# Kernel optimization log

Measured on AMD Instinct MI355X. Metric: run time of the kernel, lower is better.

The kernel has to match this reference:

```python
import jax, jax.numpy as jnp
import numpy as np

N, C, D, Q, G = 262144, 72, 256, 128, 3  # points, in_channels, hidden, queries, heads
EPS_LN = 1e-5


def _ln(x, g, b):
    m = jnp.mean(x, axis=-1, keepdims=True)
    v = jnp.mean(jnp.square(x - m), axis=-1, keepdims=True)
    return (x - m) * jax.lax.rsqrt(v + EPS_LN) * g + b


def _normalize(x):
    n = jnp.linalg.norm(x, axis=-1, keepdims=True)
    return x / jnp.maximum(n, 1e-12)


def setup_inputs() -> dict:
    key = jax.random.key(0)
    ks = iter(jax.random.split(key, 32))
    r = lambda *s: (jax.random.normal(next(ks), s, dtype=jnp.float32) * 0.02)
    inp = {
        'point_feat': jax.random.normal(next(ks), (N, C), dtype=jnp.float32),
        # input_proj: Linear(C,D) -> LN -> GELU -> Linear(D,D)
        'ip_w1': r(C, D), 'ip_b1': r(D), 'ip_ln_g': jnp.ones((D,), jnp.float32),
        'ip_ln_b': jnp.zeros((D,), jnp.float32), 'ip_w2': r(D, D), 'ip_b2': r(D),
        # point_head: LN -> Linear -> GELU -> Linear
        'ph_ln_g': jnp.ones((D,), jnp.float32), 'ph_ln_b': jnp.zeros((D,), jnp.float32),
        'ph_w1': r(D, D), 'ph_b1': r(D), 'ph_w2': r(D, D), 'ph_b2': r(D),
        # per-head params stacked on leading G axis
        'qe': r(G, Q, D),
        'qh_ln_g': jnp.ones((G, D), jnp.float32), 'qh_ln_b': jnp.zeros((G, D), jnp.float32),
        'qh_w1': r(G, D, D), 'qh_b1': r(G, D), 'qh_w2': r(G, D, D), 'qh_b2': r(G, D),
        'sh_ln_g': jnp.ones((G, D), jnp.float32), 'sh_ln_b': jnp.zeros((G, D), jnp.float32),
        'sh_w1': r(G, D, D), 'sh_b1': r(G, D), 'sh_w2': r(G, D, 1), 'sh_b2': r(G, 1),
        'logit_scale': jnp.full((G,), np.log(10.0), dtype=jnp.float32),
    }
    return inp


def reference(point_feat, ip_w1, ip_b1, ip_ln_g, ip_ln_b, ip_w2, ip_b2,
              ph_ln_g, ph_ln_b, ph_w1, ph_b1, ph_w2, ph_b2,
              qe, qh_ln_g, qh_ln_b, qh_w1, qh_b1, qh_w2, qh_b2,
              sh_ln_g, sh_ln_b, sh_w1, sh_b1, sh_w2, sh_b2, logit_scale):
    gelu = lambda x: jax.nn.gelu(x, approximate=False)  # torch nn.GELU default (erf)
    # shared trunk
    h = gelu(_ln(point_feat @ ip_w1 + ip_b1, ip_ln_g, ip_ln_b)) @ ip_w2 + ip_b2  # [N,D]
    point_embed = h + (gelu(_ln(h, ph_ln_g, ph_ln_b) @ ph_w1 + ph_b1) @ ph_w2 + ph_b2)
    # per-head query MLP (vectorized over G)
    qh = _ln(qe, qh_ln_g[:, None, :], qh_ln_b[:, None, :])
    qh = gelu(jnp.einsum('gqd,gde->gqe', qh, qh_w1) + qh_b1[:, None, :])
    query_embed = qe + jnp.einsum('gqd,gde->gqe', qh, qh_w2) + qh_b2[:, None, :]  # [G,Q,D]
    # scaled cosine-similarity cross-attention (normalize_mask_embeddings=True)
    pmask = _normalize(point_embed)                      # [N,D]
    qmask = _normalize(query_embed)                      # [G,Q,D]
    scale = jnp.exp(logit_scale)[:, None, None]
    mask_logits = scale * jnp.einsum('gqd,nd->gqn', qmask, pmask)   # [G,Q,N]
    mask_weights = jax.nn.softmax(mask_logits, axis=-1)
    pooled = jnp.einsum('gqn,nd->gqd', mask_weights, point_embed)
    refined = query_embed + pooled                       # [G,Q,D]
    # score head
    sh = _ln(refined, sh_ln_g[:, None, :], sh_ln_b[:, None, :])
    sh = gelu(jnp.einsum('gqd,gde->gqe', sh, sh_w1) + sh_b1[:, None, :])
    score_logits = (jnp.einsum('gqd,gdo->gqo', sh, sh_w2) + sh_b2[:, None, :])[..., 0]  # [G,Q]
    return point_embed, mask_logits, score_logits, refined
```

## Files before the change

kernel.cpp:

```cpp
#include <hip/hip_runtime.h>
#include <math.h>

#define NPTS 262144
#define CIN  72
#define DIM  256

typedef _Float16 h8v __attribute__((ext_vector_type(8)));
typedef _Float16 h4v __attribute__((ext_vector_type(4)));
typedef float    f4v __attribute__((ext_vector_type(4)));

__device__ __forceinline__ float gelu_erf(float x) {
    return 0.5f * x * (1.0f + erff(x * 0.70710678118654752440f));
}

__global__ void prep_kernel(const float* __restrict__ w1, const float* __restrict__ w2,
                            const float* __restrict__ p1, const float* __restrict__ p2,
                            _Float16* __restrict__ WT1, _Float16* __restrict__ WT2,
                            _Float16* __restrict__ WTp1, _Float16* __restrict__ WTp2,
                            float* __restrict__ sumexp, float* __restrict__ pooled)
{
    int idx = blockIdx.x * 256 + threadIdx.x;
    if (idx < 24576) {
        int n = idx / 96, k = idx - n * 96;
        WT1[idx] = (_Float16)(k < CIN ? w1[k * DIM + n] : 0.0f);
    } else if (idx < 24576 + 65536) {
        int t = idx - 24576; int n = t >> 8, k = t & 255;
        WT2[t] = (_Float16)w2[k * DIM + n];
    } else if (idx < 24576 + 131072) {
        int t = idx - (24576 + 65536); int n = t >> 8, k = t & 255;
        WTp1[t] = (_Float16)p1[k * DIM + n];
    } else if (idx < 24576 + 196608) {
        int t = idx - (24576 + 131072); int n = t >> 8, k = t & 255;
        WTp2[t] = (_Float16)p2[k * DIM + n];
    } else if (idx < 24576 + 196608 + 384) {
        sumexp[idx - (24576 + 196608)] = 0.0f;
    } else if (idx < 24576 + 196608 + 384 + 98304) {
        pooled[idx - (24576 + 196608 + 384)] = 0.0f;
    }
}

__device__ __forceinline__ float block_sum256(float v, float* s4) {
    #pragma unroll
    for (int off = 1; off < 64; off <<= 1) v += __shfl_xor(v, off, 64);
    __syncthreads();
    if ((threadIdx.x & 63) == 0) s4[threadIdx.x >> 6] = v;
    __syncthreads();
    return s4[0] + s4[1] + s4[2] + s4[3];
}

__global__ __launch_bounds__(256) void query_kernel(
    const float* __restrict__ qe, const float* __restrict__ qg, const float* __restrict__ qb,
    const float* __restrict__ qw1, const float* __restrict__ qb1,
    const float* __restrict__ qw2, const float* __restrict__ qb2,
    float* __restrict__ qemb, _Float16* __restrict__ qmask)
{
    __shared__ float sv[DIM], s2[DIM], s4[4];
    const int row = blockIdx.x, g = row >> 7, d = threadIdx.x;
    const float* w1 = qw1 + (size_t)g * DIM * DIM;
    const float* w2 = qw2 + (size_t)g * DIM * DIM;
    float x = qe[row * DIM + d];
    float mean = block_sum256(x, s4) * (1.0f / DIM);
    float dv = x - mean;
    float var = block_sum256(dv * dv, s4) * (1.0f / DIM);
    float y = dv * rsqrtf(var + 1e-5f) * qg[g * DIM + d] + qb[g * DIM + d];
    sv[d] = y;
    __syncthreads();
    float a1 = 0.0f;
    for (int k = 0; k < DIM; ++k) a1 += sv[k] * w1[k * DIM + d];
    a1 = gelu_erf(a1 + qb1[g * DIM + d]);
    s2[d] = a1;
    __syncthreads();
    float a2 = 0.0f;
    for (int k = 0; k < DIM; ++k) a2 += s2[k] * w2[k * DIM + d];
    float q2 = x + a2 + qb2[g * DIM + d];
    qemb[row * DIM + d] = q2;
    float ss = block_sum256(q2 * q2, s4);
    float inv = 1.0f / fmaxf(sqrtf(ss), 1e-12f);
    qmask[row * DIM + d] = (_Float16)(q2 * inv);
}

__device__ __forceinline__ void zero_acc44(f4v (&acc)[4][4]) {
    #pragma unroll
    for (int m = 0; m < 4; ++m)
        #pragma unroll
        for (int n = 0; n < 4; ++n) {
            f4v z = {0.0f, 0.0f, 0.0f, 0.0f};
            acc[m][n] = z;
        }
}

__device__ __forceinline__ void mm_tile(f4v (&acc)[4][4], const _Float16* sA,
                                        const _Float16* __restrict__ WT, int wtStride,
                                        int nKt, int cb, int l15, int lg)
{
    for (int kt = 0; kt < nKt; ++kt) {
        h8v a[4], b[4];
        #pragma unroll
        for (int m = 0; m < 4; ++m)
            a[m] = *(const h8v*)(sA + (m * 16 + l15) * 264 + kt * 32 + lg * 8);
        #pragma unroll
        for (int n = 0; n < 4; ++n)
            b[n] = *(const h8v*)(WT + (size_t)(cb + n * 16 + l15) * wtStride + kt * 32 + lg * 8);
        #pragma unroll
        for (int m = 0; m < 4; ++m)
            #pragma unroll
            for (int n = 0; n < 4; ++n)
                acc[m][n] = __builtin_amdgcn_mfma_f32_16x16x32_f16(a[m], b[n], acc[m][n], 0, 0, 0);
    }
}

__device__ __forceinline__ void ln_stats(const f4v (&acc)[4][4],
                                         float (*sRed)[64][2], float (*sStat)[2],
                                         int wv, int l15, int lg, int tid)
{
    #pragma unroll
    for (int m = 0; m < 4; ++m) {
        float s[4] = {0, 0, 0, 0}, ss[4] = {0, 0, 0, 0};
        #pragma unroll
        for (int n = 0; n < 4; ++n)
            #pragma unroll
            for (int i = 0; i < 4; ++i) { float v = acc[m][n][i]; s[i] += v; ss[i] += v * v; }
        #pragma unroll
        for (int off = 1; off < 16; off <<= 1)
            #pragma unroll
            for (int i = 0; i < 4; ++i) {
                s[i] += __shfl_xor(s[i], off, 64);
                ss[i] += __shfl_xor(ss[i], off, 64);
            }
        if (l15 == 0)
            #pragma unroll
            for (int i = 0; i < 4; ++i) {
                int r = m * 16 + lg * 4 + i;
                sRed[wv][r][0] = s[i]; sRed[wv][r][1] = ss[i];
            }
    }
    __syncthreads();
    if (tid < 64) {
        float s = 0, ss = 0;
        #pragma unroll
        for (int w = 0; w < 4; ++w) { s += sRed[w][tid][0]; ss += sRed[w][tid][1]; }
        float mean = s * (1.0f / 256.0f);
        float var = ss * (1.0f / 256.0f) - mean * mean;
        sStat[tid][0] = mean;
        sStat[tid][1] = rsqrtf(var + 1e-5f);
    }
    __syncthreads();
}

__global__ __launch_bounds__(256, 2) void trunk_kernel(
    const float* __restrict__ pf,
    const float* __restrict__ ib1, const float* __restrict__ ig, const float* __restrict__ ibb,
    const float* __restrict__ ib2,
    const float* __restrict__ pg, const float* __restrict__ pb,
    const float* __restrict__ pb1, const float* __restrict__ pb2,
    const _Float16* __restrict__ WT1, const _Float16* __restrict__ WT2,
    const _Float16* __restrict__ WTp1, const _Float16* __restrict__ WTp2,
    float* __restrict__ peo, float* __restrict__ inv_norm, _Float16* __restrict__ peT)
{
    __shared__ __align__(16) _Float16 sAct[64][264];
    __shared__ float sRed[4][64][2];
    __shared__ float sStat[64][2];

    const int tid = threadIdx.x;
    const int wv = tid >> 6, ln = tid & 63, l15 = ln & 15, lg = ln >> 4;
    const int cb = wv * 64;
    const int rowbase = blockIdx.x * 64;

    for (int idx = tid; idx < 64 * 96; idx += 256) {
        int r = idx / 96, c = idx - r * 96;
        sAct[r][c] = (_Float16)(c < CIN ? pf[(size_t)(rowbase + r) * CIN + c] : 0.0f);
    }
    __syncthreads();

    f4v acc[4][4];
    float h4[4][4][4];

    zero_acc44(acc);
    mm_tile(acc, &sAct[0][0], WT1, 96, 3, cb, l15, lg);
    {
        float bc[4], gc[4], bb[4];
        #pragma unroll
        for (int n = 0; n < 4; ++n) {
            int col = cb + n * 16 + l15;
            bc[n] = ib1[col]; gc[n] = ig[col]; bb[n] = ibb[col];
        }
        #pragma unroll
        for (int m = 0; m < 4; ++m)
            #pragma unroll
            for (int n = 0; n < 4; ++n)
                #pragma unroll
                for (int i = 0; i < 4; ++i) acc[m][n][i] += bc[n];
        ln_stats(acc, sRed, sStat, wv, l15, lg, tid);
        #pragma unroll
        for (int m = 0; m < 4; ++m)
            #pragma unroll
            for (int i = 0; i < 4; ++i) {
                int r = m * 16 + lg * 4 + i;
                float mean = sStat[r][0], rstd = sStat[r][1];
                #pragma unroll
                for (int n = 0; n < 4; ++n) {
                    float v = (acc[m][n][i] - mean) * rstd * gc[n] + bb[n];
                    sAct[r][cb + n * 16 + l15] = (_Float16)gelu_erf(v);
                }
            }
    }
    __syncthreads();

    zero_acc44(acc);
    mm_tile(acc, &sAct[0][0], WT2, 256, 8, cb, l15, lg);
    {
        float bc[4], gc[4], bb[4];
        #pragma unroll
        for (int n = 0; n < 4; ++n) {
            int col = cb + n * 16 + l15;
            bc[n] = ib2[col]; gc[n] = pg[col]; bb[n] = pb[col];
        }
        #pragma unroll
        for (int m = 0; m < 4; ++m)
            #pragma unroll
            for (int n = 0; n < 4; ++n)
                #pragma unroll
                for (int i = 0; i < 4; ++i) {
                    float h = acc[m][n][i] + bc[n];
                    h4[m][n][i] = h;
                    acc[m][n][i] = h;
                }
        ln_stats(acc, sRed, sStat, wv, l15, lg, tid);
        #pragma unroll
        for (int m = 0; m < 4; ++m)
            #pragma unroll
            for (int i = 0; i < 4; ++i) {
                int r = m * 16 + lg * 4 + i;
                float mean = sStat[r][0], rstd = sStat[r][1];
                #pragma unroll
                for (int n = 0; n < 4; ++n) {
                    float v = (h4[m][n][i] - mean) * rstd * gc[n] + bb[n];
                    sAct[r][cb + n * 16 + l15] = (_Float16)v;
                }
            }
    }
    __syncthreads();

    zero_acc44(acc);
    mm_tile(acc, &sAct[0][0], WTp1, 256, 8, cb, l15, lg);
    __syncthreads();
    {
        float bc[4];
        #pragma unroll
        for (int n = 0; n < 4; ++n) bc[n] = pb1[cb + n * 16 + l15];
        #pragma unroll
        for (int m = 0; m < 4; ++m)
            #pragma unroll
            for (int i = 0; i < 4; ++i) {
                int r = m * 16 + lg * 4 + i;
                #pragma unroll
                for (int n = 0; n < 4; ++n) {
                    float v = gelu_erf(acc[m][n][i] + bc[n]);
                    sAct[r][cb + n * 16 + l15] = (_Float16)v;
                }
            }
    }
    __syncthreads();

    zero_acc44(acc);
    mm_tile(acc, &sAct[0][0], WTp2, 256, 8, cb, l15, lg);
    {
        float bc[4];
        #pragma unroll
        for (int n = 0; n < 4; ++n) bc[n] = pb2[cb + n * 16 + l15];
        #pragma unroll
        for (int m = 0; m < 4; ++m)
            #pragma unroll
            for (int n = 0; n < 4; ++n)
                #pragma unroll
                for (int i = 0; i < 4; ++i)
                    acc[m][n][i] += bc[n] + h4[m][n][i];
        #pragma unroll
        for (int m = 0; m < 4; ++m) {
            float ss[4] = {0, 0, 0, 0};
            #pragma unroll
            for (int n = 0; n < 4; ++n)
                #pragma unroll
                for (int i = 0; i < 4; ++i) { float v = acc[m][n][i]; ss[i] += v * v; }
            #pragma unroll
            for (int off = 1; off < 16; off <<= 1)
                #pragma unroll
                for (int i = 0; i < 4; ++i) ss[i] += __shfl_xor(ss[i], off, 64);
            if (l15 == 0)
                #pragma unroll
                for (int i = 0; i < 4; ++i) sRed[wv][m * 16 + lg * 4 + i][0] = ss[i];
        }
        __syncthreads();
        if (tid < 64) {
            float ss = 0;
            #pragma unroll
            for (int w = 0; w < 4; ++w) ss += sRed[w][tid][0];
            float inv = 1.0f / fmaxf(sqrtf(ss), 1e-12f);
            sStat[tid][0] = inv;
            inv_norm[rowbase + tid] = inv;
        }
        __syncthreads();
        #pragma unroll
        for (int m = 0; m < 4; ++m)
            #pragma unroll
            for (int n = 0; n < 4; ++n) {
                int col = cb + n * 16 + l15;
                h4v pk;
                #pragma unroll
                for (int i = 0; i < 4; ++i) {
                    int r = m * 16 + lg * 4 + i;
                    float v = acc[m][n][i];
                    peo[(size_t)(rowbase + r) * DIM + col] = v;
                    pk[i] = (_Float16)v;
                }
                *(h4v*)(peT + (size_t)col * NPTS + rowbase + m * 16 + lg * 4) = pk;
            }
    }
}

__global__ __launch_bounds__(256, 2) void logits_kernel(
    const _Float16* __restrict__ qmask, const float* __restrict__ peo,
    const float* __restrict__ inv_norm, const float* __restrict__ lsc,
    float* __restrict__ ml, float* __restrict__ sumexp)
{
    const int tid = threadIdx.x;
    const int wv = tid >> 6, ln = tid & 63, l15 = ln & 15, lg = ln >> 4;
    const int nb = blockIdx.x * 64;
    const int mb = wv * 96;

    f4v acc[6][4];
    #pragma unroll
    for (int m = 0; m < 6; ++m)
        #pragma unroll
        for (int n = 0; n < 4; ++n) { f4v z = {0, 0, 0, 0}; acc[m][n] = z; }

    float inv[4];
    #pragma unroll
    for (int n = 0; n < 4; ++n) inv[n] = inv_norm[nb + n * 16 + l15];

    for (int kt = 0; kt < 8; ++kt) {
        h8v a[6], b[4];
        #pragma unroll
        for (int n = 0; n < 4; ++n) {
            const float* p = peo + (size_t)(nb + n * 16 + l15) * DIM + kt * 32 + lg * 8;
            float4 u0 = *(const float4*)p;
            float4 u1 = *(const float4*)(p + 4);
            h8v t;
            t[0] = (_Float16)(u0.x * inv[n]); t[1] = (_Float16)(u0.y * inv[n]);
            t[2] = (_Float16)(u0.z * inv[n]); t[3] = (_Float16)(u0.w * inv[n]);
            t[4] = (_Float16)(u1.x * inv[n]); t[5] = (_Float16)(u1.y * inv[n]);
            t[6] = (_Float16)(u1.z * inv[n]); t[7] = (_Float16)(u1.w * inv[n]);
            b[n] = t;
        }
        #pragma unroll
        for (int m = 0; m < 6; ++m)
            a[m] = *(const h8v*)(qmask + (size_t)(mb + m * 16 + l15) * DIM + kt * 32 + lg * 8);
        #pragma unroll
        for (int m = 0; m < 6; ++m)
            #pragma unroll
            for (int n = 0; n < 4; ++n)
                acc[m][n] = __builtin_amdgcn_mfma_f32_16x16x32_f16(a[m], b[n], acc[m][n], 0, 0, 0);
    }

    #pragma unroll
    for (int m = 0; m < 6; ++m) {
        int g = (mb + m * 16) >> 7;
        float sc = expf(lsc[g]);
        float es[4] = {0, 0, 0, 0};
        #pragma unroll
        for (int n = 0; n < 4; ++n)
            #pragma unroll
            for (int i = 0; i < 4; ++i) {
                int row = mb + m * 16 + lg * 4 + i;
                int col = nb + n * 16 + l15;
                float v = acc[m][n][i] * sc;
                ml[(size_t)row * NPTS + col] = v;
                es[i] += __expf(v);
            }
        #pragma unroll
        for (int off = 1; off < 16; off <<= 1)
            #pragma unroll
            for (int i = 0; i < 4; ++i) es[i] += __shfl_xor(es[i], off, 64);
        if (l15 == 0)
            #pragma unroll
            for (int i = 0; i < 4; ++i)
                atomicAdd(&sumexp[mb + m * 16 + lg * 4 + i], es[i]);
    }
}

__global__ __launch_bounds__(512, 2) void pooled_kernel(
    const float* __restrict__ ml, const _Float16* __restrict__ peT,
    float* __restrict__ pooled)
{
    const int tid = threadIdx.x;
    const int wv = tid >> 6, ln = tid & 63, l15 = ln & 15, lg = ln >> 4;
    const int mt = blockIdx.x >> 7, kc = blockIdx.x & 127;
    const int mb = mt * 192 + (wv & 3) * 48;
    const int cbv = (wv >> 2) * 128;
    const size_t kb = (size_t)kc * 2048;

    f4v acc[3][8];
    #pragma unroll
    for (int m = 0; m < 3; ++m)
        #pragma unroll
        for (int n = 0; n < 8; ++n) { f4v z = {0, 0, 0, 0}; acc[m][n] = z; }

    for (int ks = 0; ks < 64; ++ks) {
        size_t k0 = kb + ks * 32 + lg * 8;
        h8v a[3];
        #pragma unroll
        for (int m = 0; m < 3; ++m) {
            const float* p = ml + (size_t)(mb + m * 16 + l15) * NPTS + k0;
            float4 u0 = *(const float4*)p;
            float4 u1 = *(const float4*)(p + 4);
            h8v t;
            t[0] = (_Float16)__expf(u0.x); t[1] = (_Float16)__expf(u0.y);
            t[2] = (_Float16)__expf(u0.z); t[3] = (_Float16)__expf(u0.w);
            t[4] = (_Float16)__expf(u1.x); t[5] = (_Float16)__expf(u1.y);
            t[6] = (_Float16)__expf(u1.z); t[7] = (_Float16)__expf(u1.w);
            a[m] = t;
        }
        h8v b[8];
        #pragma unroll
        for (int n = 0; n < 8; ++n)
            b[n] = *(const h8v*)(peT + (size_t)(cbv + n * 16 + l15) * NPTS + k0);
        #pragma unroll
        for (int m = 0; m < 3; ++m)
            #pragma unroll
            for (int n = 0; n < 8; ++n)
                acc[m][n] = __builtin_amdgcn_mfma_f32_16x16x32_f16(a[m], b[n], acc[m][n], 0, 0, 0);
    }
    #pragma unroll
    for (int m = 0; m < 3; ++m)
        #pragma unroll
        for (int n = 0; n < 8; ++n)
            #pragma unroll
            for (int i = 0; i < 4; ++i)
                atomicAdd(&pooled[(mb + m * 16 + lg * 4 + i) * DIM + cbv + n * 16 + l15],
                          acc[m][n][i]);
}

__global__ __launch_bounds__(256) void finalize_kernel(
    const float* __restrict__ pooled, const float* __restrict__ sumexp,
    const float* __restrict__ qemb,
    const float* __restrict__ sg, const float* __restrict__ sb,
    const float* __restrict__ sw1, const float* __restrict__ sb1,
    const float* __restrict__ sw2, const float* __restrict__ sb2,
    float* __restrict__ rf, float* __restrict__ sl)
{
    __shared__ float sv[DIM], s4[4];
    const int row = blockIdx.x, g = row >> 7, d = threadIdx.x;
    float r = qemb[row * DIM + d] + pooled[row * DIM + d] / sumexp[row];
    rf[row * DIM + d] = r;
    float mean = block_sum256(r, s4) * (1.0f / DIM);
    float dv = r - mean;
    float var = block_sum256(dv * dv, s4) * (1.0f / DIM);
    float y = dv * rsqrtf(var + 1e-5f) * sg[g * DIM + d] + sb[g * DIM + d];
    sv[d] = y;
    __syncthreads();
    const float* w1 = sw1 + (size_t)g * DIM * DIM;
    float a1 = 0.0f;
    for (int k = 0; k < DIM; ++k) a1 += sv[k] * w1[k * DIM + d];
    a1 = gelu_erf(a1 + sb1[g * DIM + d]);
    float part = a1 * sw2[g * DIM + d];
    float tot = block_sum256(part, s4);
    if (d == 0) sl[row] = tot + sb2[g];
}

extern "C" void kernel_launch(void* const* d_in, const int* in_sizes, int n_in,
                              void* d_out, int out_size, void* d_ws, size_t ws_size,
                              hipStream_t stream) {
    const float* pf       = (const float*)d_in[0];
    const float* ip_w1    = (const float*)d_in[1];
    const float* ip_b1    = (const float*)d_in[2];
    const float* ip_ln_g  = (const float*)d_in[3];
    const float* ip_ln_b  = (const float*)d_in[4];
    const float* ip_w2    = (const float*)d_in[5];
    const float* ip_b2    = (const float*)d_in[6];
    const float* ph_ln_g  = (const float*)d_in[7];
    const float* ph_ln_b  = (const float*)d_in[8];
    const float* ph_w1    = (const float*)d_in[9];
    const float* ph_b1    = (const float*)d_in[10];
    const float* ph_w2    = (const float*)d_in[11];
    const float* ph_b2    = (const float*)d_in[12];
    const float* qe       = (const float*)d_in[13];
    const float* qh_ln_g  = (const float*)d_in[14];
    const float* qh_ln_b  = (const float*)d_in[15];
    const float* qh_w1    = (const float*)d_in[16];
    const float* qh_b1    = (const float*)d_in[17];
    const float* qh_w2    = (const float*)d_in[18];
    const float* qh_b2    = (const float*)d_in[19];
    const float* sh_ln_g  = (const float*)d_in[20];
    const float* sh_ln_b  = (const float*)d_in[21];
    const float* sh_w1    = (const float*)d_in[22];
    const float* sh_b1    = (const float*)d_in[23];
    const float* sh_w2    = (const float*)d_in[24];
    const float* sh_b2    = (const float*)d_in[25];
    const float* lsc      = (const float*)d_in[26];

    float* out = (float*)d_out;
    float* pe_out = out;
    float* ml     = out + 67108864LL;
    float* sl     = out + 167772160LL;
    float* rf     = out + 167772544LL;

    char* ws = (char*)d_ws;
    _Float16* WT1   = (_Float16*)(ws + 0);
    _Float16* WT2   = (_Float16*)(ws + 49152);
    _Float16* WTp1  = (_Float16*)(ws + 180224);
    _Float16* WTp2  = (_Float16*)(ws + 311296);
    _Float16* qmask = (_Float16*)(ws + 442368);
    float*    qemb  = (float*)(ws + 638976);
    float*    sume  = (float*)(ws + 1032192);
    float*    pool  = (float*)(ws + 1033728);
    float*    invn  = (float*)(ws + 1426944);
    _Float16* peT   = (_Float16*)(ws + 2475520);

    prep_kernel<<<1250, 256, 0, stream>>>(ip_w1, ip_w2, ph_w1, ph_w2,
                                          WT1, WT2, WTp1, WTp2, sume, pool);
    query_kernel<<<384, 256, 0, stream>>>(qe, qh_ln_g, qh_ln_b, qh_w1, qh_b1,
                                          qh_w2, qh_b2, qemb, qmask);
    trunk_kernel<<<4096, 256, 0, stream>>>(pf, ip_b1, ip_ln_g, ip_ln_b, ip_b2,
                                           ph_ln_g, ph_ln_b, ph_b1, ph_b2,
                                           WT1, WT2, WTp1, WTp2, pe_out, invn, peT);
    logits_kernel<<<4096, 256, 0, stream>>>(qmask, pe_out, invn, lsc, ml, sume);
    pooled_kernel<<<256, 512, 0, stream>>>(ml, peT, pool);
    finalize_kernel<<<384, 256, 0, stream>>>(pool, sume, qemb, sh_ln_g, sh_ln_b,
                                             sh_w1, sh_b1, sh_w2, sh_b2, rf, sl);
}
```

Before: 2.132 ms.

## Precompute fp16 normalized point embeddings, prefetch operands, retune trunk and pooled kernels

The trunk kernel now also writes a half-precision copy of the normalized point embedding, when the workspace is large enough, so the logits kernel reads fp16 instead of fp32 data and skips the per-element scaling. It relies on sStat[r][0] holding the inverse norm at that point in the trunk kernel. Both the logits and pooled kernels now register-prefetch the next K-slice, and the pooled kernel uses twice as many blocks with half the K range each, which doubles the atomic reductions. The trunk kernel also gets vectorized input loading, a higher occupancy hint and fp16 storage of the residual, which trades register pressure against residual precision. Small query and finalize loops are unrolled.

```diff
diff --git a/kernel.cpp b/kernel.cpp
--- a/kernel.cpp
+++ b/kernel.cpp
@@ -66,11 +66,13 @@
     sv[d] = y;
     __syncthreads();
     float a1 = 0.0f;
+    #pragma unroll 8
     for (int k = 0; k < DIM; ++k) a1 += sv[k] * w1[k * DIM + d];
     a1 = gelu_erf(a1 + qb1[g * DIM + d]);
     s2[d] = a1;
     __syncthreads();
     float a2 = 0.0f;
+    #pragma unroll 8
     for (int k = 0; k < DIM; ++k) a2 += s2[k] * w2[k * DIM + d];
     float q2 = x + a2 + qb2[g * DIM + d];
     qemb[row * DIM + d] = q2;
@@ -147,7 +149,7 @@
     __syncthreads();
 }
 
-__global__ __launch_bounds__(256, 2) void trunk_kernel(
+__global__ __launch_bounds__(256, 4) void trunk_kernel(
     const float* __restrict__ pf,
     const float* __restrict__ ib1, const float* __restrict__ ig, const float* __restrict__ ibb,
     const float* __restrict__ ib2,
@@ -155,7 +157,8 @@
     const float* __restrict__ pb1, const float* __restrict__ pb2,
     const _Float16* __restrict__ WT1, const _Float16* __restrict__ WT2,
     const _Float16* __restrict__ WTp1, const _Float16* __restrict__ WTp2,
-    float* __restrict__ peo, float* __restrict__ inv_norm, _Float16* __restrict__ peT)
+    float* __restrict__ peo, float* __restrict__ inv_norm, _Float16* __restrict__ peT,
+    _Float16* __restrict__ pmH)
 {
     __shared__ __align__(16) _Float16 sAct[64][264];
     __shared__ float sRed[4][64][2];
@@ -166,14 +169,21 @@
     const int cb = wv * 64;
     const int rowbase = blockIdx.x * 64;
 
-    for (int idx = tid; idx < 64 * 96; idx += 256) {
-        int r = idx / 96, c = idx - r * 96;
-        sAct[r][c] = (_Float16)(c < CIN ? pf[(size_t)(rowbase + r) * CIN + c] : 0.0f);
+    for (int idx = tid; idx < 1152; idx += 256) {
+        int r = idx / 18, c4 = idx - r * 18;
+        float4 u = *(const float4*)(pf + (size_t)(rowbase + r) * CIN + c4 * 4);
+        h4v h; h[0] = (_Float16)u.x; h[1] = (_Float16)u.y; h[2] = (_Float16)u.z; h[3] = (_Float16)u.w;
+        *(h4v*)(&sAct[r][c4 * 4]) = h;
+    }
+    for (int idx = tid; idx < 384; idx += 256) {
+        int r = idx / 6, c4 = idx - r * 6;
+        h4v z = {};
+        *(h4v*)(&sAct[r][72 + c4 * 4]) = z;
     }
     __syncthreads();
 
     f4v acc[4][4];
-    float h4[4][4][4];
+    h4v h16[4][4];
 
     zero_acc44(acc);
     mm_tile(acc, &sAct[0][0], WT1, 96, 3, cb, l15, lg);
@@ -222,8 +232,8 @@
                 #pragma unroll
                 for (int i = 0; i < 4; ++i) {
                     float h = acc[m][n][i] + bc[n];
-                    h4[m][n][i] = h;
                     acc[m][n][i] = h;
+                    h16[m][n][i] = (_Float16)h;
                 }
         ln_stats(acc, sRed, sStat, wv, l15, lg, tid);
         #pragma unroll
@@ -234,7 +244,7 @@
                 float mean = sStat[r][0], rstd = sStat[r][1];
                 #pragma unroll
                 for (int n = 0; n < 4; ++n) {
-                    float v = (h4[m][n][i] - mean) * rstd * gc[n] + bb[n];
+                    float v = (acc[m][n][i] - mean) * rstd * gc[n] + bb[n];
                     sAct[r][cb + n * 16 + l15] = (_Float16)v;
                 }
             }
@@ -274,7 +284,7 @@
             for (int n = 0; n < 4; ++n)
                 #pragma unroll
                 for (int i = 0; i < 4; ++i)
-                    acc[m][n][i] += bc[n] + h4[m][n][i];
+                    acc[m][n][i] += bc[n] + (float)h16[m][n][i];
         #pragma unroll
         for (int m = 0; m < 4; ++m) {
             float ss[4] = {0, 0, 0, 0};
@@ -311,6 +321,7 @@
                     int r = m * 16 + lg * 4 + i;
                     float v = acc[m][n][i];
                     peo[(size_t)(rowbase + r) * DIM + col] = v;
+                    if (pmH) pmH[(size_t)(rowbase + r) * DIM + col] = (_Float16)(v * sStat[r][0]);
                     pk[i] = (_Float16)v;
                 }
                 *(h4v*)(peT + (size_t)col * NPTS + rowbase + m * 16 + lg * 4) = pk;
@@ -318,9 +329,11 @@
     }
 }
 
+template<bool PM>
 __global__ __launch_bounds__(256, 2) void logits_kernel(
-    const _Float16* __restrict__ qmask, const float* __restrict__ peo,
-    const float* __restrict__ inv_norm, const float* __restrict__ lsc,
+    const _Float16* __restrict__ qmask, const _Float16* __restrict__ pmH,
+    const float* __restrict__ peo, const float* __restrict__ inv_norm,
+    const float* __restrict__ lsc,
     float* __restrict__ ml, float* __restrict__ sumexp)
 {
     const int tid = threadIdx.x;
@@ -335,23 +348,37 @@
         for (int n = 0; n < 4; ++n) { f4v z = {0, 0, 0, 0}; acc[m][n] = z; }
 
     float inv[4];
-    #pragma unroll
-    for (int n = 0; n < 4; ++n) inv[n] = inv_norm[nb + n * 16 + l15];
-
+    if constexpr (!PM) {
+        #pragma unroll
+        for (int n = 0; n < 4; ++n) inv[n] = inv_norm[nb + n * 16 + l15];
+    }
+
+    auto loadB = [&](int kt, h8v (&b)[4]) {
+        #pragma unroll
+        for (int n = 0; n < 4; ++n) {
+            if constexpr (PM) {
+                b[n] = *(const h8v*)(pmH + (size_t)(nb + n * 16 + l15) * DIM + kt * 32 + lg * 8);
+            } else {
+                const float* p = peo + (size_t)(nb + n * 16 + l15) * DIM + kt * 32 + lg * 8;
+                float4 u0 = *(const float4*)p;
+                float4 u1 = *(const float4*)(p + 4);
+                h8v t;
+                t[0] = (_Float16)(u0.x * inv[n]); t[1] = (_Float16)(u0.y * inv[n]);
+                t[2] = (_Float16)(u0.z * inv[n]); t[3] = (_Float16)(u0.w * inv[n]);
+                t[4] = (_Float16)(u1.x * inv[n]); t[5] = (_Float16)(u1.y * inv[n]);
+                t[6] = (_Float16)(u1.z * inv[n]); t[7] = (_Float16)(u1.w * inv[n]);
+                b[n] = t;
+            }
+        }
+    };
+
+    h8v b0[4];
+    loadB(0, b0);
+    #pragma unroll
     for (int kt = 0; kt < 8; ++kt) {
-        h8v a[6], b[4];
-        #pragma unroll
-        for (int n = 0; n < 4; ++n) {
-            const float* p = peo + (size_t)(nb + n * 16 + l15) * DIM + kt * 32 + lg * 8;
-            float4 u0 = *(const float4*)p;
-            float4 u1 = *(const float4*)(p + 4);
-            h8v t;
-            t[0] = (_Float16)(u0.x * inv[n]); t[1] = (_Float16)(u0.y * inv[n]);
-            t[2] = (_Float16)(u0.z * inv[n]); t[3] = (_Float16)(u0.w * inv[n]);
-            t[4] = (_Float16)(u1.x * inv[n]); t[5] = (_Float16)(u1.y * inv[n]);
-            t[6] = (_Float16)(u1.z * inv[n]); t[7] = (_Float16)(u1.w * inv[n]);
-            b[n] = t;
-        }
+        h8v b1[4];
+        if (kt < 7) loadB(kt + 1, b1);
+        h8v a[6];
         #pragma unroll
         for (int m = 0; m < 6; ++m)
             a[m] = *(const h8v*)(qmask + (size_t)(mb + m * 16 + l15) * DIM + kt * 32 + lg * 8);
@@ -359,7 +386,11 @@
         for (int m = 0; m < 6; ++m)
             #pragma unroll
             for (int n = 0; n < 4; ++n)
-                acc[m][n] = __builtin_amdgcn_mfma_f32_16x16x32_f16(a[m], b[n], acc[m][n], 0, 0, 0);
+                acc[m][n] = __builtin_amdgcn_mfma_f32_16x16x32_f16(a[m], b0[n], acc[m][n], 0, 0, 0);
+        if (kt < 7) {
+            #pragma unroll
+            for (int n = 0; n < 4; ++n) b0[n] = b1[n];
+        }
     }
 
     #pragma unroll
@@ -394,10 +425,10 @@
 {
     const int tid = threadIdx.x;
     const int wv = tid >> 6, ln = tid & 63, l15 = ln & 15, lg = ln >> 4;
-    const int mt = blockIdx.x >> 7, kc = blockIdx.x & 127;
-    const int mb = mt * 192 + (wv & 3) * 48;
-    const int cbv = (wv >> 2) * 128;
-    const size_t kb = (size_t)kc * 2048;
+    const int qs = blockIdx.x >> 8, kc = blockIdx.x & 255;
+    const int rb = qs * 192 + (wv & 3) * 48;
+    const int db = (wv >> 2) * 128;
+    const size_t kb = (size_t)kc * 1024;
 
     f4v acc[3][8];
     #pragma unroll
@@ -405,38 +436,55 @@
         #pragma unroll
         for (int n = 0; n < 8; ++n) { f4v z = {0, 0, 0, 0}; acc[m][n] = z; }
 
-    for (int ks = 0; ks < 64; ++ks) {
-        size_t k0 = kb + ks * 32 + lg * 8;
-        h8v a[3];
+    auto loadA = [&](int ks, f4v (&a)[6]) {
         #pragma unroll
         for (int m = 0; m < 3; ++m) {
-            const float* p = ml + (size_t)(mb + m * 16 + l15) * NPTS + k0;
-            float4 u0 = *(const float4*)p;
-            float4 u1 = *(const float4*)(p + 4);
+            const float* p = ml + (size_t)(rb + m * 16 + l15) * NPTS + kb + ks * 32 + lg * 8;
+            a[2 * m]     = *(const f4v*)p;
+            a[2 * m + 1] = *(const f4v*)(p + 4);
+        }
+    };
+    auto loadB = [&](int ks, h8v (&b)[8]) {
+        #pragma unroll
+        for (int n = 0; n < 8; ++n)
+            b[n] = *(const h8v*)(peT + (size_t)(db + n * 16 + l15) * NPTS + kb + ks * 32 + lg * 8);
+    };
+
+    f4v a0[6]; h8v b0[8];
+    loadA(0, a0); loadB(0, b0);
+    for (int ks = 0; ks < 32; ++ks) {
+        f4v a1[6]; h8v b1[8];
+        if (ks < 31) { loadA(ks + 1, a1); loadB(ks + 1, b1); }
+        h8v pa[3];
+        #pragma unroll
+        for (int m = 0; m < 3; ++m) {
             h8v t;
-            t[0] = (_Float16)__expf(u0.x); t[1] = (_Float16)__expf(u0.y);
-            t[2] = (_Float16)__expf(u0.z); t[3] = (_Float16)__expf(u0.w);
-            t[4] = (_Float16)__expf(u1.x); t[5] = (_Float16)__expf(u1.y);
-            t[6] = (_Float16)__expf(u1.z); t[7] = (_Float16)__expf(u1.w);
-            a[m] = t;
-        }
-        h8v b[8];
+            #pragma unroll
+            for (int j = 0; j < 4; ++j) {
+                t[j]     = (_Float16)__expf(a0[2 * m][j]);
+                t[4 + j] = (_Float16)__expf(a0[2 * m + 1][j]);
+            }
+            pa[m] = t;
+        }
+        #pragma unroll
+        for (int m = 0; m < 3; ++m)
+            #pragma unroll
+            for (int n = 0; n < 8; ++n)
+                acc[m][n] = __builtin_amdgcn_mfma_f32_16x16x32_f16(pa[m], b0[n], acc[m][n], 0, 0, 0);
+        if (ks < 31) {
+            #pragma unroll
+            for (int i = 0; i < 6; ++i) a0[i] = a1[i];
+            #pragma unroll
+            for (int n = 0; n < 8; ++n) b0[n] = b1[n];
+        }
+    }
+    #pragma unroll
+    for (int m = 0; m < 3; ++m)
         #pragma unroll
         for (int n = 0; n < 8; ++n)
-            b[n] = *(const h8v*)(peT + (size_t)(cbv + n * 16 + l15) * NPTS + k0);
-        #pragma unroll
-        for (int m = 0; m < 3; ++m)
-            #pragma unroll
-            for (int n = 0; n < 8; ++n)
-                acc[m][n] = __builtin_amdgcn_mfma_f32_16x16x32_f16(a[m], b[n], acc[m][n], 0, 0, 0);
-    }
-    #pragma unroll
-    for (int m = 0; m < 3; ++m)
-        #pragma unroll
-        for (int n = 0; n < 8; ++n)
             #pragma unroll
             for (int i = 0; i < 4; ++i)
-                atomicAdd(&pooled[(mb + m * 16 + lg * 4 + i) * DIM + cbv + n * 16 + l15],
+                atomicAdd(&pooled[(size_t)(rb + m * 16 + lg * 4 + i) * DIM + db + n * 16 + l15],
                           acc[m][n][i]);
 }
 
@@ -460,6 +508,7 @@
     __syncthreads();
     const float* w1 = sw1 + (size_t)g * DIM * DIM;
     float a1 = 0.0f;
+    #pragma unroll 8
     for (int k = 0; k < DIM; ++k) a1 += sv[k] * w1[k * DIM + d];
     a1 = gelu_erf(a1 + sb1[g * DIM + d]);
     float part = a1 * sw2[g * DIM + d];
@@ -514,7 +563,12 @@
     float*    sume  = (float*)(ws + 1032192);
     float*    pool  = (float*)(ws + 1033728);
     float*    invn  = (float*)(ws + 1426944);
-    _Float16* peT   = (_Float16*)(ws + 2475520);
+
+    const size_t PM_BYTES = 134217728ULL;
+    bool big = ws_size >= (2475520ULL + 2 * PM_BYTES);
+    _Float16* pmH = big ? (_Float16*)(ws + 2475520) : (_Float16*)nullptr;
+    _Float16* peT = big ? (_Float16*)(ws + 2475520 + PM_BYTES)
+                        : (_Float16*)(ws + 2475520);
 
     prep_kernel<<<1250, 256, 0, stream>>>(ip_w1, ip_w2, ph_w1, ph_w2,
                                           WT1, WT2, WTp1, WTp2, sume, pool);
@@ -522,9 +576,12 @@
                                           qh_w2, qh_b2, qemb, qmask);
     trunk_kernel<<<4096, 256, 0, stream>>>(pf, ip_b1, ip_ln_g, ip_ln_b, ip_b2,
                                            ph_ln_g, ph_ln_b, ph_b1, ph_b2,
-                                           WT1, WT2, WTp1, WTp2, pe_out, invn, peT);
-    logits_kernel<<<4096, 256, 0, stream>>>(qmask, pe_out, invn, lsc, ml, sume);
-    pooled_kernel<<<256, 512, 0, stream>>>(ml, peT, pool);
+                                           WT1, WT2, WTp1, WTp2, pe_out, invn, peT, pmH);
+    if (big)
+        logits_kernel<true><<<4096, 256, 0, stream>>>(qmask, pmH, pe_out, invn, lsc, ml, sume);
+    else
+        logits_kernel<false><<<4096, 256, 0, stream>>>(qmask, pmH, pe_out, invn, lsc, ml, sume);
+    pooled_kernel<<<512, 512, 0, stream>>>(ml, peT, pool);
     finalize_kernel<<<384, 256, 0, stream>>>(pool, sume, qemb, sh_ln_g, sh_ln_b,
                                              sh_w1, sh_b1, sh_w2, sh_b2, rf, sl);
 }
```

Result: faster. 2.071 ms (-2.9%).
